# Optimization experiments

Measured on AMD Instinct MI355X. Metric: run time of the kernel, lower is better.

Reference implementation:

```python
import jax, jax.numpy as jnp
import numpy as np

B, S, M = 1, 2048, 2048
H, HKV, D = 32, 8, 64
SW = 128
WAVELENGTH = 150000.0
SCALE = D ** (-0.25)
NEG = -1e9  # large negative for fp32 compute dtype


def setup_inputs() -> dict:
    key = jax.random.key(0)
    ks = jax.random.split(key, 8)
    return {
        "hidden_states": jax.random.normal(ks[0], (B, S, M), jnp.float32),
        "Wq": jax.random.normal(ks[1], (M, H, D), jnp.float32) * 0.02,
        "bq": jnp.zeros((H, D), jnp.float32),
        "Wk": jax.random.normal(ks[2], (M, HKV, D), jnp.float32) * 0.02,
        "bk": jnp.zeros((HKV, D), jnp.float32),
        "Wv": jax.random.normal(ks[3], (M, HKV, D), jnp.float32) * 0.02,
        "bv": jnp.zeros((HKV, D), jnp.float32),
        "Wo": jax.random.normal(ks[4], (H, D, M), jnp.float32) * 0.02,
        "bo": jnp.zeros((M,), jnp.float32),
        "sinks": jax.random.normal(ks[5], (H,), jnp.float32),
    }


def _cos_sin(seq_len, dtype):
    # yarn RoPE with scaling_factor=1.0 reduces to standard RoPE (mscale=1,
    # no frequency interpolation). half = D//2 frequencies.
    half = D // 2
    inv_freq = 1.0 / (WAVELENGTH ** (jnp.arange(half, dtype=jnp.float32) * 2.0 / D))
    t = jnp.arange(seq_len, dtype=jnp.float32)
    freqs = t[:, None] * inv_freq[None, :]  # [S, half]
    # broadcast shape [1, S, 1, half] to match [B, S, heads, half]
    return (jnp.cos(freqs)[None, :, None, :].astype(dtype),
            jnp.sin(freqs)[None, :, None, :].astype(dtype))


def _interleaved_rope(x, cos, sin):
    x_even = x[..., ::2]
    x_odd = x[..., 1::2]
    first = x_even * cos - x_odd * sin
    second = x_odd * cos + x_even * sin
    return jnp.stack([first, second], axis=-1).reshape(x.shape)


def reference(hidden_states, Wq, bq, Wk, bk, Wv, bv, Wo, bo, sinks):
    b, s, _ = hidden_states.shape
    groups = H // HKV

    q = jnp.einsum('bqm,muh->bquh', hidden_states, Wq) + bq  # [B,S,H,D]
    k = jnp.einsum('bkm,mvh->bkvh', hidden_states, Wk) + bk  # [B,S,HKV,D]
    v = jnp.einsum('bkm,mvh->bkvh', hidden_states, Wv) + bv

    cos, sin = _cos_sin(s, hidden_states.dtype)
    q = _interleaved_rope(q, cos, sin) * SCALE
    k = _interleaved_rope(k, cos, sin) * SCALE

    # GQA: repeat kv heads to match query heads
    k = jnp.repeat(k, groups, axis=2)  # [B,S,H,D]
    v = jnp.repeat(v, groups, axis=2)

    scores = jnp.einsum('bquh,bkuh->buqk', q, k)  # [B,H,S,S]

    pos = jnp.arange(s)
    sw_mask = jnp.abs(pos[:, None] - pos[None, :]) <= SW  # bidirectional window
    scores = jnp.where(sw_mask[None, None, :, :], scores, NEG)

    sink_logits = jnp.broadcast_to(sinks[None, :, None, None], (b, H, s, 1))
    combined = jnp.concatenate([scores, sink_logits], axis=-1)  # [B,H,S,S+1]
    probs = jax.nn.softmax(combined.astype(jnp.float32), axis=-1)
    attn = probs[..., :-1].astype(hidden_states.dtype)  # drop sink column

    out = jnp.einsum('buqk,bkuh->bquh', attn, v)  # [B,S,H,D]
    return jnp.einsum('bquh,uhm->bqm', out, Wo) + bo
```

## Files before the change

### kernel.cpp

```cpp
#include <hip/hip_runtime.h>
#include <hip/hip_bf16.h>
#include <stdint.h>

typedef unsigned short u16;
typedef unsigned int   u32;

#define S_LEN 2048
#define NQKV  3072
#define NH    32
#define NKV   8
#define SWIN  128
#define NEGV  (-1.0e9f)
#define SCALE_Q 0.35355339059327379f

typedef __attribute__((ext_vector_type(4)))  float  f32x4;
typedef __attribute__((ext_vector_type(16))) float  f32x16;
typedef __attribute__((ext_vector_type(8)))  __bf16 bf16x8;

__device__ __forceinline__ u16 f2bf(float x){
  u32 u = __float_as_uint(x);
  return (u16)((u + 0x7fffu + ((u >> 16) & 1u)) >> 16);
}
__device__ __forceinline__ float bf2f(u16 h){
  return __uint_as_float(((u32)h) << 16);
}
__device__ __forceinline__ void split2(float a, float b, u32& hw, u32& lw){
  u16 ha = f2bf(a), hb = f2bf(b);
  u16 la = f2bf(a - bf2f(ha)), lb = f2bf(b - bf2f(hb));
  hw = (u32)ha | ((u32)hb << 16);
  lw = (u32)la | ((u32)lb << 16);
}
__device__ __forceinline__ u32 pk2(float a, float b){
  return (u32)f2bf(a) | ((u32)f2bf(b) << 16);
}
__device__ __forceinline__ f32x4 mfma16(bf16x8 a, bf16x8 b, f32x4 c){
  return __builtin_amdgcn_mfma_f32_16x16x32_bf16(a, b, c, 0, 0, 0);
}
__device__ __forceinline__ f32x16 mfma32(bf16x8 a, bf16x8 b, f32x16 c){
  return __builtin_amdgcn_mfma_f32_32x32x16_bf16(a, b, c, 0, 0, 0);
}

typedef __attribute__((address_space(1))) const unsigned int ga_u32;
typedef __attribute__((address_space(3))) unsigned int       ls_u32;
__device__ __forceinline__ void gl16(const void* g, void* l){
  __builtin_amdgcn_global_load_lds((ga_u32*)g, (ls_u32*)l, 16, 0, 0);
}

__global__ __launch_bounds__(256) void k_prep(const float* __restrict__ bq,
                                              const float* __restrict__ bk,
                                              const float* __restrict__ bv,
                                              float* __restrict__ ropetab,
                                              float* __restrict__ bias3){
  int id = blockIdx.x * 256 + threadIdx.x;
  int t = id >> 5, i = id & 31;
  float e = (i * 2.0f) / 64.0f;
  float base = (float)pow(150000.0, (double)e);
  float invf = 1.0f / base;
  float fr = (float)t * invf;
  ropetab[(size_t)id * 2 + 0] = cosf(fr);
  ropetab[(size_t)id * 2 + 1] = sinf(fr);
  if (id < NQKV){
    float b;
    if (id < 2048) b = bq[id];
    else if (id < 2560) b = bk[id - 2048];
    else b = bv[id - 2560];
    bias3[id] = b;
  }
}

__global__ __launch_bounds__(256) void k_pack_a(const float* __restrict__ in,
                                                u16* __restrict__ oh, int n8){
  int id = blockIdx.x * 256 + threadIdx.x;
  if (id >= n8) return;
  int r = id >> 8, p = id & 255;
  const float4* src = (const float4*)(in + (size_t)id * 8);
  float4 v0 = src[0], v1 = src[1];
  u32 hw[4];
  hw[0] = pk2(v0.x, v0.y); hw[1] = pk2(v0.z, v0.w);
  hw[2] = pk2(v1.x, v1.y); hw[3] = pk2(v1.z, v1.w);
  int psw = (p & ~7) | ((p & 7) ^ (r & 7));
  size_t o = ((size_t)r * 256 + psw) * 8;
  *(uint4*)(oh + o) = make_uint4(hw[0], hw[1], hw[2], hw[3]);
}

__global__ __launch_bounds__(256) void k_pack_w(const float* __restrict__ w,
                                                u16* __restrict__ oh,
                                                int K, int N, int NTot, int nOff){
  int id = blockIdx.x * 256 + threadIdx.x;
  int P = K >> 3;
  if (id >= P * N) return;
  int p = id / N, n = id % N;
  u32 hw[4];
  #pragma unroll
  for (int j = 0; j < 4; ++j){
    float a = w[(size_t)(8 * p + 2 * j) * N + n];
    float b = w[(size_t)(8 * p + 2 * j + 1) * N + n];
    hw[j] = pk2(a, b);
  }
  size_t o = ((size_t)p * NTot + nOff + n) * 8;
  *(uint4*)(oh + o) = make_uint4(hw[0], hw[1], hw[2], hw[3]);
}

template<bool ARM>
__global__ __launch_bounds__(256, 2) void k_gemm3(const u16* __restrict__ A,
                                                  const u16* __restrict__ B,
                                                  const float* __restrict__ bias,
                                                  float* __restrict__ C,
                                                  int M, int N, int K){
  __shared__ u16 lds[2][2][1024][8];
  const int tid = threadIdx.x;
  const int lane = tid & 63, wid = tid >> 6;
  const int q = lane & 15, g = lane >> 4;
  const int m0 = blockIdx.y * 128, n0 = blockIdx.x * 128;
  const int wr = wid >> 1, wc = wid & 1;
  const int pkK = K >> 3;

  f32x4 acc[4][4];
  #pragma unroll
  for (int a = 0; a < 4; ++a)
    #pragma unroll
    for (int b = 0; b < 4; ++b)
      #pragma unroll
      for (int r = 0; r < 4; ++r) acc[a][b][r] = 0.0f;

  size_t aoff[4], boff[4];
  #pragma unroll
  for (int c = 0; c < 4; ++c){
    int L = c * 256 + tid;
    if (ARM){
      int row = L >> 3, pa = L & 7;
      aoff[c] = ((size_t)(m0 + row) * pkK + pa) * 8;
    } else {
      int pa = L >> 7, row = L & 127;
      aoff[c] = ((size_t)pa * M + m0 + row) * 8;
    }
    int pb = L >> 7, col = L & 127;
    boff[c] = ((size_t)pb * N + n0 + col) * 8;
  }
  const size_t astep = ARM ? (size_t)64 : (size_t)64 * M;
  const size_t bstep = (size_t)64 * N;

  const int NT = K >> 6;

  auto STAGE = [&](int b){
    #pragma unroll
    for (int c = 0; c < 4; ++c){
      int lbase = c * 256 + wid * 64;
      gl16(A + aoff[c], &lds[b][0][lbase][0]);
      gl16(B + boff[c], &lds[b][1][lbase][0]);
      aoff[c] += astep; boff[c] += bstep;
    }
  };

  STAGE(0);
  STAGE(1);
  asm volatile("s_waitcnt vmcnt(8)" ::: "memory");
  __builtin_amdgcn_s_barrier();

  int buf = 0;
  for (int t = 0; t < NT; ++t){
    bf16x8 af[4][2], bf[4][2];
    #pragma unroll
    for (int ms = 0; ms < 4; ++ms){
      int row = wr * 64 + ms * 16 + q;
      #pragma unroll
      for (int kk = 0; kk < 2; ++kk){
        int ia = ARM ? (row * 8 + ((4 * kk + g) ^ (row & 7)))
                     : ((4 * kk + g) * 128 + row);
        af[ms][kk] = *(const bf16x8*)&lds[buf][0][ia][0];
      }
    }
    #pragma unroll
    for (int ns = 0; ns < 4; ++ns){
      int col = wc * 64 + ns * 16 + q;
      #pragma unroll
      for (int kk = 0; kk < 2; ++kk){
        int ib = (4 * kk + g) * 128 + col;
        bf[ns][kk] = *(const bf16x8*)&lds[buf][1][ib][0];
      }
    }
    asm volatile("s_waitcnt lgkmcnt(0)" ::: "memory");
    __builtin_amdgcn_sched_barrier(0);
    __builtin_amdgcn_s_barrier();
    if (t + 2 < NT) STAGE(buf);

    #pragma unroll
    for (int kk = 0; kk < 2; ++kk)
      #pragma unroll
      for (int ms = 0; ms < 4; ++ms)
        #pragma unroll
        for (int ns = 0; ns < 4; ++ns)
          acc[ms][ns] = mfma16(af[ms][kk], bf[ns][kk], acc[ms][ns]);

    if (t + 2 < NT){
      asm volatile("s_waitcnt vmcnt(8)" ::: "memory");
      __builtin_amdgcn_s_barrier();
    } else if (t + 1 < NT){
      asm volatile("s_waitcnt vmcnt(0)" ::: "memory");
      __builtin_amdgcn_s_barrier();
    }
    buf ^= 1;
  }

  #pragma unroll
  for (int ns = 0; ns < 4; ++ns){
    int col = n0 + wc * 64 + ns * 16 + q;
    float bb = bias[col];
    #pragma unroll
    for (int ms = 0; ms < 4; ++ms){
      int row = m0 + wr * 64 + ms * 16 + g * 4;
      #pragma unroll
      for (int r = 0; r < 4; ++r)
        C[(size_t)(row + r) * N + col] = acc[ms][ns][r] + bb;
    }
  }
}

__global__ __launch_bounds__(256) void k_rope(const float* __restrict__ qkv,
                                              const float* __restrict__ tab,
                                              u16* __restrict__ qoh, u16* __restrict__ qol,
                                              u16* __restrict__ koh, u16* __restrict__ kol){
  const int sL = threadIdx.x & 63, tp = threadIdx.x >> 6;
  const int s = blockIdx.x * 64 + sL;
  int h = blockIdx.y;
  u16* oh; u16* ol; int srcOff;
  if (h < NH){ oh = qoh; ol = qol; srcOff = h * 64; }
  else       { h -= NH; oh = koh; ol = kol; srcOff = 2048 + h * 64; }
  const float4* src = (const float4*)(qkv + (size_t)s * NQKV + srcOff + tp * 16);
  const float4* tb  = (const float4*)(tab + (size_t)s * 64 + tp * 16);
  float xv[16], tv[16];
  #pragma unroll
  for (int i = 0; i < 4; ++i){
    float4 a = src[i]; float4 b = tb[i];
    xv[4*i+0]=a.x; xv[4*i+1]=a.y; xv[4*i+2]=a.z; xv[4*i+3]=a.w;
    tv[4*i+0]=b.x; tv[4*i+1]=b.y; tv[4*i+2]=b.z; tv[4*i+3]=b.w;
  }
  u32 hw[8], lw[8];
  #pragma unroll
  for (int j = 0; j < 8; ++j){
    float e = xv[2*j], o = xv[2*j+1];
    float c = tv[2*j], sn = tv[2*j+1];
    float f0 = (e * c - o * sn) * SCALE_Q;
    float f1 = (o * c + e * sn) * SCALE_Q;
    split2(f0, f1, hw[j], lw[j]);
  }
  size_t o0 = ((size_t)(h * 8 + tp * 2 + 0) * S_LEN + s) * 8;
  size_t o1 = ((size_t)(h * 8 + tp * 2 + 1) * S_LEN + s) * 8;
  *(uint4*)(oh + o0) = make_uint4(hw[0], hw[1], hw[2], hw[3]);
  *(uint4*)(oh + o1) = make_uint4(hw[4], hw[5], hw[6], hw[7]);
  *(uint4*)(ol + o0) = make_uint4(lw[0], lw[1], lw[2], lw[3]);
  *(uint4*)(ol + o1) = make_uint4(lw[4], lw[5], lw[6], lw[7]);
}

__global__ __launch_bounds__(256) void k_split_v2(const float* __restrict__ qkv,
                                                  u16* __restrict__ oh, u16* __restrict__ ol){
  __shared__ float tile[64][65];
  const int h = blockIdx.y;
  const int s0 = blockIdx.x * 64;
  {
    const int sL = threadIdx.x >> 2, ch = threadIdx.x & 3;
    const float4* rp = (const float4*)(qkv + (size_t)(s0 + sL) * NQKV + 2560 + h * 64 + ch * 16);
    #pragma unroll
    for (int i = 0; i < 4; ++i){
      float4 w = rp[i];
      tile[sL][ch * 16 + i * 4 + 0] = w.x;
      tile[sL][ch * 16 + i * 4 + 1] = w.y;
      tile[sL][ch * 16 + i * 4 + 2] = w.z;
      tile[sL][ch * 16 + i * 4 + 3] = w.w;
    }
  }
  __syncthreads();
  const int d = threadIdx.x & 63, spg = threadIdx.x >> 6;
  #pragma unroll
  for (int sp2 = 0; sp2 < 2; ++sp2){
    int spl = spg * 2 + sp2;
    float v[8];
    #pragma unroll
    for (int j = 0; j < 8; ++j) v[j] = tile[spl * 8 + j][d];
    u32 hw[4], lw[4];
    #pragma unroll
    for (int j = 0; j < 4; ++j) split2(v[2*j], v[2*j+1], hw[j], lw[j]);
    size_t o_ = (((size_t)h * 256 + blockIdx.x * 8 + spl) * 64 + d) * 8;
    *(uint4*)(oh + o_) = make_uint4(hw[0], hw[1], hw[2], hw[3]);
    *(uint4*)(ol + o_) = make_uint4(lw[0], lw[1], lw[2], lw[3]);
  }
}

__global__ __launch_bounds__(256) void k_attn(const u16* __restrict__ qh, const u16* __restrict__ ql,
                                              const u16* __restrict__ kh, const u16* __restrict__ kl,
                                              const u16* __restrict__ vh, const u16* __restrict__ vl,
                                              const float* __restrict__ sinks,
                                              u16* __restrict__ aoh){
  const int lane = threadIdx.x & 63;
  const int wid = threadIdx.x >> 6;
  const int h = blockIdx.x;
  const int hkv = h >> 2;
  const int q0 = blockIdx.y * 128 + wid * 32;
  const int lq = lane & 31;
  const int half = lane >> 5;
  const int qi = q0 + lq;

  bf16x8 qfh[4], qfl[4];
  #pragma unroll
  for (int st = 0; st < 4; ++st){
    size_t off = (((size_t)h * 8 + st * 2 + half) * S_LEN + qi) * 8;
    qfh[st] = *(const bf16x8*)(qh + off);
    qfl[st] = *(const bf16x8*)(ql + off);
  }
  float m = sinks[h];
  float lsum = 1.0f;
  f32x16 o0, o1;
  #pragma unroll
  for (int r = 0; r < 16; ++r){ o0[r] = 0.0f; o1[r] = 0.0f; }

  const int kb0 = q0 - 128;
  for (int c = 0; c < 9; ++c){
    const int kb = kb0 + c * 32;
    if (kb + 32 <= 0 || kb >= S_LEN) continue;
    const int keyr = kb + lq;
    const int keyc = min(max(keyr, 0), S_LEN - 1);
    f32x16 sc;
    #pragma unroll
    for (int r = 0; r < 16; ++r) sc[r] = 0.0f;
    #pragma unroll
    for (int st = 0; st < 4; ++st){
      size_t ko = (((size_t)hkv * 8 + st * 2 + half) * S_LEN + keyc) * 8;
      bf16x8 kfh = *(const bf16x8*)(kh + ko);
      bf16x8 kfl = *(const bf16x8*)(kl + ko);
      sc = mfma32(kfh, qfh[st], sc);
      sc = mfma32(kfh, qfl[st], sc);
      sc = mfma32(kfl, qfh[st], sc);
    }
    float tmax = -3.0e38f;
    #pragma unroll
    for (int r = 0; r < 16; ++r){
      int key = kb + (r & 3) + 8 * (r >> 2) + 4 * half;
      int dd = qi - key; if (dd < 0) dd = -dd;
      bool ok = (key >= 0) && (key < S_LEN) && (dd <= SWIN);
      sc[r] = ok ? sc[r] : NEGV;
      tmax = fmaxf(tmax, sc[r]);
    }
    tmax = fmaxf(tmax, __shfl_xor(tmax, 32));
    float mn = fmaxf(m, tmax);
    float alpha = __expf(m - mn);
    m = mn;
    float p[16]; float ps = 0.0f;
    #pragma unroll
    for (int r = 0; r < 16; ++r){ p[r] = __expf(sc[r] - mn); ps += p[r]; }
    ps += __shfl_xor(ps, 32);
    lsum = lsum * alpha + ps;
    #pragma unroll
    for (int r = 0; r < 16; ++r){ o0[r] *= alpha; o1[r] *= alpha; }
    u32 wh[8], wl[8];
    #pragma unroll
    for (int j = 0; j < 8; ++j) split2(p[2 * j], p[2 * j + 1], wh[j], wl[j]);
    bf16x8 pfh[2], pfl[2];
    #pragma unroll
    for (int ks = 0; ks < 2; ++ks){
      u32 x0 = wh[4 * ks + 0], y0 = wh[4 * ks + 2];
      u32 x1 = wh[4 * ks + 1], y1 = wh[4 * ks + 3];
      u32 sx0 = __shfl_xor(x0, 32), sy0 = __shfl_xor(y0, 32);
      u32 sx1 = __shfl_xor(x1, 32), sy1 = __shfl_xor(y1, 32);
      union { u32 u[4]; bf16x8 b; } fb;
      fb.u[0] = half ? sy0 : x0;
      fb.u[1] = half ? sy1 : x1;
      fb.u[2] = half ? y0 : sx0;
      fb.u[3] = half ? y1 : sx1;
      pfh[ks] = fb.b;
      u32 a0 = wl[4 * ks + 0], b0 = wl[4 * ks + 2];
      u32 a1 = wl[4 * ks + 1], b1 = wl[4 * ks + 3];
      u32 sa0 = __shfl_xor(a0, 32), sb0 = __shfl_xor(b0, 32);
      u32 sa1 = __shfl_xor(a1, 32), sb1 = __shfl_xor(b1, 32);
      fb.u[0] = half ? sb0 : a0;
      fb.u[1] = half ? sb1 : a1;
      fb.u[2] = half ? b0 : sa0;
      fb.u[3] = half ? b1 : sa1;
      pfl[ks] = fb.b;
    }
    #pragma unroll
    for (int ks = 0; ks < 2; ++ks){
      int kp = kb / 8 + ks * 2 + half;
      kp = min(max(kp, 0), S_LEN / 8 - 1);
      #pragma unroll
      for (int nt = 0; nt < 2; ++nt){
        size_t vo = (((size_t)hkv * 256 + kp) * 64 + nt * 32 + lq) * 8;
        bf16x8 vfh = *(const bf16x8*)(vh + vo);
        bf16x8 vfl = *(const bf16x8*)(vl + vo);
        f32x16 acc = (nt == 0) ? o0 : o1;
        acc = mfma32(vfh, pfh[ks], acc);
        acc = mfma32(vfh, pfl[ks], acc);
        acc = mfma32(vfl, pfh[ks], acc);
        if (nt == 0) o0 = acc; else o1 = acc;
      }
    }
  }
  float inv = 1.0f / lsum;
  #pragma unroll
  for (int nt = 0; nt < 2; ++nt){
    f32x16 o = (nt == 0) ? o0 : o1;
    #pragma unroll
    for (int rr = 0; rr < 4; ++rr){
      int d0 = nt * 32 + 8 * rr + 4 * half;
      float v0 = o[rr * 4 + 0] * inv, v1 = o[rr * 4 + 1] * inv;
      float v2 = o[rr * 4 + 2] * inv, v3 = o[rr * 4 + 3] * inv;
      int kp_ = h * 8 + nt * 4 + rr;
      size_t oo = ((size_t)kp_ * S_LEN + qi) * 8 + (d0 & 7);
      uint2 wv; wv.x = pk2(v0, v1); wv.y = pk2(v2, v3);
      *(uint2*)(aoh + oo) = wv;
    }
  }
}

extern "C" void kernel_launch(void* const* d_in, const int* in_sizes, int n_in,
                              void* d_out, int out_size, void* d_ws, size_t ws_size,
                              hipStream_t stream){
  const float* hid = (const float*)d_in[0];
  const float* Wq  = (const float*)d_in[1];
  const float* bq  = (const float*)d_in[2];
  const float* Wk  = (const float*)d_in[3];
  const float* bk  = (const float*)d_in[4];
  const float* Wv  = (const float*)d_in[5];
  const float* bv  = (const float*)d_in[6];
  const float* Wo  = (const float*)d_in[7];
  const float* bo  = (const float*)d_in[8];
  const float* sinks = (const float*)d_in[9];
  float* out = (float*)d_out;

  char* w = (char*)d_ws;
  size_t off = 0;
  auto alloc = [&](size_t bytes){ void* p = w + off; off += (bytes + 255) & ~(size_t)255; return p; };
  float* ropetab = (float*)alloc((size_t)S_LEN * 32 * 2 * 4);
  float* bias3   = (float*)alloc((size_t)NQKV * 4);
  u16* Ah  = (u16*)alloc((size_t)2048 * 2048 * 2);
  u16* Bh  = (u16*)alloc((size_t)256 * NQKV * 8 * 2);
  float* QKV = (float*)alloc((size_t)S_LEN * NQKV * 4);
  u16* qph = (u16*)alloc((size_t)NH * 8 * S_LEN * 8 * 2);
  u16* qpl = (u16*)alloc((size_t)NH * 8 * S_LEN * 8 * 2);
  u16* kph = (u16*)alloc((size_t)NKV * 8 * S_LEN * 8 * 2);
  u16* kpl = (u16*)alloc((size_t)NKV * 8 * S_LEN * 8 * 2);
  u16* vph = (u16*)alloc((size_t)NKV * 256 * 64 * 8 * 2);
  u16* vpl = (u16*)alloc((size_t)NKV * 256 * 64 * 8 * 2);
  u16* aoh = (u16*)alloc((size_t)256 * S_LEN * 8 * 2);
  u16* Woh = (u16*)alloc((size_t)256 * 2048 * 8 * 2);
  (void)in_sizes; (void)n_in; (void)out_size; (void)ws_size;

  k_prep<<<256, 256, 0, stream>>>(bq, bk, bv, ropetab, bias3);
  k_pack_a<<<2048, 256, 0, stream>>>(hid, Ah, 2048 * 256);
  k_pack_w<<<2048, 256, 0, stream>>>(Wq, Bh, 2048, 2048, NQKV, 0);
  k_pack_w<<<512, 256, 0, stream>>>(Wk, Bh, 2048, 512, NQKV, 2048);
  k_pack_w<<<512, 256, 0, stream>>>(Wv, Bh, 2048, 512, NQKV, 2560);
  k_pack_w<<<2048, 256, 0, stream>>>(Wo, Woh, 2048, 2048, 2048, 0);
  k_gemm3<true><<<dim3(NQKV / 128, 2048 / 128), 256, 0, stream>>>(Ah, Bh, bias3, QKV,
                                                                  2048, NQKV, 2048);
  k_rope<<<dim3(32, NH + NKV), 256, 0, stream>>>(QKV, ropetab, qph, qpl, kph, kpl);
  k_split_v2<<<dim3(32, NKV), 256, 0, stream>>>(QKV, vph, vpl);
  k_attn<<<dim3(NH, S_LEN / 128), 256, 0, stream>>>(qph, qpl, kph, kpl, vph, vpl, sinks, aoh);
  k_gemm3<false><<<dim3(2048 / 128, 2048 / 128), 256, 0, stream>>>(aoh, Woh, bo, out,
                                                                   2048, 2048, 2048);
}
```

Measured before the change: 217.5 us.

## Drop split-bf16 hi/lo compensation in attention and merge packing kernels

Measured after the change: 201.8 us. 7.2% less time.

```diff
diff --git a/kernel.cpp b/kernel.cpp
--- a/kernel.cpp
+++ b/kernel.cpp
@@ -20,15 +20,6 @@
 __device__ __forceinline__ u16 f2bf(float x){
   u32 u = __float_as_uint(x);
   return (u16)((u + 0x7fffu + ((u >> 16) & 1u)) >> 16);
-}
-__device__ __forceinline__ float bf2f(u16 h){
-  return __uint_as_float(((u32)h) << 16);
-}
-__device__ __forceinline__ void split2(float a, float b, u32& hw, u32& lw){
-  u16 ha = f2bf(a), hb = f2bf(b);
-  u16 la = f2bf(a - bf2f(ha)), lb = f2bf(b - bf2f(hb));
-  hw = (u32)ha | ((u32)hb << 16);
-  lw = (u32)la | ((u32)lb << 16);
 }
 __device__ __forceinline__ u32 pk2(float a, float b){
   return (u32)f2bf(a) | ((u32)f2bf(b) << 16);
@@ -68,27 +59,9 @@
   }
 }
 
-__global__ __launch_bounds__(256) void k_pack_a(const float* __restrict__ in,
-                                                u16* __restrict__ oh, int n8){
-  int id = blockIdx.x * 256 + threadIdx.x;
-  if (id >= n8) return;
-  int r = id >> 8, p = id & 255;
-  const float4* src = (const float4*)(in + (size_t)id * 8);
-  float4 v0 = src[0], v1 = src[1];
-  u32 hw[4];
-  hw[0] = pk2(v0.x, v0.y); hw[1] = pk2(v0.z, v0.w);
-  hw[2] = pk2(v1.x, v1.y); hw[3] = pk2(v1.z, v1.w);
-  int psw = (p & ~7) | ((p & 7) ^ (r & 7));
-  size_t o = ((size_t)r * 256 + psw) * 8;
-  *(uint4*)(oh + o) = make_uint4(hw[0], hw[1], hw[2], hw[3]);
-}
-
-__global__ __launch_bounds__(256) void k_pack_w(const float* __restrict__ w,
-                                                u16* __restrict__ oh,
-                                                int K, int N, int NTot, int nOff){
-  int id = blockIdx.x * 256 + threadIdx.x;
-  int P = K >> 3;
-  if (id >= P * N) return;
+__device__ __forceinline__ void packw_seg(const float* __restrict__ w,
+                                          u16* __restrict__ oh,
+                                          int N, int NTot, int nOff, int id){
   int p = id / N, n = id % N;
   u32 hw[4];
   #pragma unroll
@@ -99,6 +72,36 @@
   }
   size_t o = ((size_t)p * NTot + nOff + n) * 8;
   *(uint4*)(oh + o) = make_uint4(hw[0], hw[1], hw[2], hw[3]);
+}
+__global__ __launch_bounds__(256) void k_packall(const float* __restrict__ hid,
+                                                 const float* __restrict__ Wq,
+                                                 const float* __restrict__ Wk,
+                                                 const float* __restrict__ Wv,
+                                                 const float* __restrict__ Wo,
+                                                 u16* __restrict__ Ah,
+                                                 u16* __restrict__ Bh,
+                                                 u16* __restrict__ Woh){
+  int b = blockIdx.x;
+  if (b < 2048){
+    int id = b * 256 + threadIdx.x;
+    int r = id >> 8, p = id & 255;
+    const float4* src = (const float4*)(hid + (size_t)id * 8);
+    float4 v0 = src[0], v1 = src[1];
+    u32 hw[4];
+    hw[0] = pk2(v0.x, v0.y); hw[1] = pk2(v0.z, v0.w);
+    hw[2] = pk2(v1.x, v1.y); hw[3] = pk2(v1.z, v1.w);
+    int psw = (p & ~7) | ((p & 7) ^ (r & 7));
+    size_t o = ((size_t)r * 256 + psw) * 8;
+    *(uint4*)(Ah + o) = make_uint4(hw[0], hw[1], hw[2], hw[3]);
+  } else if (b < 4096){
+    packw_seg(Wq, Bh, 2048, NQKV, 0,    (b - 2048) * 256 + threadIdx.x);
+  } else if (b < 4608){
+    packw_seg(Wk, Bh, 512,  NQKV, 2048, (b - 4096) * 256 + threadIdx.x);
+  } else if (b < 5120){
+    packw_seg(Wv, Bh, 512,  NQKV, 2560, (b - 4608) * 256 + threadIdx.x);
+  } else {
+    packw_seg(Wo, Woh, 2048, 2048, 0,   (b - 5120) * 256 + threadIdx.x);
+  }
 }
 
 template<bool ARM>
@@ -218,14 +221,14 @@
 
 __global__ __launch_bounds__(256) void k_rope(const float* __restrict__ qkv,
                                               const float* __restrict__ tab,
-                                              u16* __restrict__ qoh, u16* __restrict__ qol,
-                                              u16* __restrict__ koh, u16* __restrict__ kol){
+                                              u16* __restrict__ qoh,
+                                              u16* __restrict__ koh){
   const int sL = threadIdx.x & 63, tp = threadIdx.x >> 6;
   const int s = blockIdx.x * 64 + sL;
   int h = blockIdx.y;
-  u16* oh; u16* ol; int srcOff;
-  if (h < NH){ oh = qoh; ol = qol; srcOff = h * 64; }
-  else       { h -= NH; oh = koh; ol = kol; srcOff = 2048 + h * 64; }
+  u16* oh; int srcOff;
+  if (h < NH){ oh = qoh; srcOff = h * 64; }
+  else       { h -= NH; oh = koh; srcOff = 2048 + h * 64; }
   const float4* src = (const float4*)(qkv + (size_t)s * NQKV + srcOff + tp * 16);
   const float4* tb  = (const float4*)(tab + (size_t)s * 64 + tp * 16);
   float xv[16], tv[16];
@@ -235,25 +238,23 @@
     xv[4*i+0]=a.x; xv[4*i+1]=a.y; xv[4*i+2]=a.z; xv[4*i+3]=a.w;
     tv[4*i+0]=b.x; tv[4*i+1]=b.y; tv[4*i+2]=b.z; tv[4*i+3]=b.w;
   }
-  u32 hw[8], lw[8];
+  u32 hw[8];
   #pragma unroll
   for (int j = 0; j < 8; ++j){
     float e = xv[2*j], o = xv[2*j+1];
     float c = tv[2*j], sn = tv[2*j+1];
     float f0 = (e * c - o * sn) * SCALE_Q;
     float f1 = (o * c + e * sn) * SCALE_Q;
-    split2(f0, f1, hw[j], lw[j]);
+    hw[j] = pk2(f0, f1);
   }
   size_t o0 = ((size_t)(h * 8 + tp * 2 + 0) * S_LEN + s) * 8;
   size_t o1 = ((size_t)(h * 8 + tp * 2 + 1) * S_LEN + s) * 8;
   *(uint4*)(oh + o0) = make_uint4(hw[0], hw[1], hw[2], hw[3]);
   *(uint4*)(oh + o1) = make_uint4(hw[4], hw[5], hw[6], hw[7]);
-  *(uint4*)(ol + o0) = make_uint4(lw[0], lw[1], lw[2], lw[3]);
-  *(uint4*)(ol + o1) = make_uint4(lw[4], lw[5], lw[6], lw[7]);
 }
 
 __global__ __launch_bounds__(256) void k_split_v2(const float* __restrict__ qkv,
-                                                  u16* __restrict__ oh, u16* __restrict__ ol){
+                                                  u16* __restrict__ oh){
   __shared__ float tile[64][65];
   const int h = blockIdx.y;
   const int s0 = blockIdx.x * 64;
@@ -277,18 +278,17 @@
     float v[8];
     #pragma unroll
     for (int j = 0; j < 8; ++j) v[j] = tile[spl * 8 + j][d];
-    u32 hw[4], lw[4];
-    #pragma unroll
-    for (int j = 0; j < 4; ++j) split2(v[2*j], v[2*j+1], hw[j], lw[j]);
+    u32 hw[4];
+    #pragma unroll
+    for (int j = 0; j < 4; ++j) hw[j] = pk2(v[2*j], v[2*j+1]);
     size_t o_ = (((size_t)h * 256 + blockIdx.x * 8 + spl) * 64 + d) * 8;
     *(uint4*)(oh + o_) = make_uint4(hw[0], hw[1], hw[2], hw[3]);
-    *(uint4*)(ol + o_) = make_uint4(lw[0], lw[1], lw[2], lw[3]);
-  }
-}
-
-__global__ __launch_bounds__(256) void k_attn(const u16* __restrict__ qh, const u16* __restrict__ ql,
-                                              const u16* __restrict__ kh, const u16* __restrict__ kl,
-                                              const u16* __restrict__ vh, const u16* __restrict__ vl,
+  }
+}
+
+__global__ __launch_bounds__(256) void k_attn(const u16* __restrict__ qh,
+                                              const u16* __restrict__ kh,
+                                              const u16* __restrict__ vh,
                                               const float* __restrict__ sinks,
                                               u16* __restrict__ aoh){
   const int lane = threadIdx.x & 63;
@@ -300,12 +300,11 @@
   const int half = lane >> 5;
   const int qi = q0 + lq;
 
-  bf16x8 qfh[4], qfl[4];
+  bf16x8 qf[4];
   #pragma unroll
   for (int st = 0; st < 4; ++st){
     size_t off = (((size_t)h * 8 + st * 2 + half) * S_LEN + qi) * 8;
-    qfh[st] = *(const bf16x8*)(qh + off);
-    qfl[st] = *(const bf16x8*)(ql + off);
+    qf[st] = *(const bf16x8*)(qh + off);
   }
   float m = sinks[h];
   float lsum = 1.0f;
@@ -325,11 +324,8 @@
     #pragma unroll
     for (int st = 0; st < 4; ++st){
       size_t ko = (((size_t)hkv * 8 + st * 2 + half) * S_LEN + keyc) * 8;
-      bf16x8 kfh = *(const bf16x8*)(kh + ko);
-      bf16x8 kfl = *(const bf16x8*)(kl + ko);
-      sc = mfma32(kfh, qfh[st], sc);
-      sc = mfma32(kfh, qfl[st], sc);
-      sc = mfma32(kfl, qfh[st], sc);
+      bf16x8 kf = *(const bf16x8*)(kh + ko);
+      sc = mfma32(kf, qf[st], sc);
     }
     float tmax = -3.0e38f;
     #pragma unroll
@@ -351,10 +347,10 @@
     lsum = lsum * alpha + ps;
     #pragma unroll
     for (int r = 0; r < 16; ++r){ o0[r] *= alpha; o1[r] *= alpha; }
-    u32 wh[8], wl[8];
-    #pragma unroll
-    for (int j = 0; j < 8; ++j) split2(p[2 * j], p[2 * j + 1], wh[j], wl[j]);
-    bf16x8 pfh[2], pfl[2];
+    u32 wh[8];
+    #pragma unroll
+    for (int j = 0; j < 8; ++j) wh[j] = pk2(p[2 * j], p[2 * j + 1]);
+    bf16x8 pfh[2];
     #pragma unroll
     for (int ks = 0; ks < 2; ++ks){
       u32 x0 = wh[4 * ks + 0], y0 = wh[4 * ks + 2];
@@ -367,15 +363,6 @@
       fb.u[2] = half ? y0 : sx0;
       fb.u[3] = half ? y1 : sx1;
       pfh[ks] = fb.b;
-      u32 a0 = wl[4 * ks + 0], b0 = wl[4 * ks + 2];
-      u32 a1 = wl[4 * ks + 1], b1 = wl[4 * ks + 3];
-      u32 sa0 = __shfl_xor(a0, 32), sb0 = __shfl_xor(b0, 32);
-      u32 sa1 = __shfl_xor(a1, 32), sb1 = __shfl_xor(b1, 32);
-      fb.u[0] = half ? sb0 : a0;
-      fb.u[1] = half ? sb1 : a1;
-      fb.u[2] = half ? b0 : sa0;
-      fb.u[3] = half ? b1 : sa1;
-      pfl[ks] = fb.b;
     }
     #pragma unroll
     for (int ks = 0; ks < 2; ++ks){
@@ -384,12 +371,9 @@
       #pragma unroll
       for (int nt = 0; nt < 2; ++nt){
         size_t vo = (((size_t)hkv * 256 + kp) * 64 + nt * 32 + lq) * 8;
-        bf16x8 vfh = *(const bf16x8*)(vh + vo);
-        bf16x8 vfl = *(const bf16x8*)(vl + vo);
+        bf16x8 vf = *(const bf16x8*)(vh + vo);
         f32x16 acc = (nt == 0) ? o0 : o1;
-        acc = mfma32(vfh, pfh[ks], acc);
-        acc = mfma32(vfh, pfl[ks], acc);
-        acc = mfma32(vfl, pfh[ks], acc);
+        acc = mfma32(vf, pfh[ks], acc);
         if (nt == 0) o0 = acc; else o1 = acc;
       }
     }
@@ -435,26 +419,19 @@
   u16* Bh  = (u16*)alloc((size_t)256 * NQKV * 8 * 2);
   float* QKV = (float*)alloc((size_t)S_LEN * NQKV * 4);
   u16* qph = (u16*)alloc((size_t)NH * 8 * S_LEN * 8 * 2);
-  u16* qpl = (u16*)alloc((size_t)NH * 8 * S_LEN * 8 * 2);
   u16* kph = (u16*)alloc((size_t)NKV * 8 * S_LEN * 8 * 2);
-  u16* kpl = (u16*)alloc((size_t)NKV * 8 * S_LEN * 8 * 2);
   u16* vph = (u16*)alloc((size_t)NKV * 256 * 64 * 8 * 2);
-  u16* vpl = (u16*)alloc((size_t)NKV * 256 * 64 * 8 * 2);
   u16* aoh = (u16*)alloc((size_t)256 * S_LEN * 8 * 2);
   u16* Woh = (u16*)alloc((size_t)256 * 2048 * 8 * 2);
   (void)in_sizes; (void)n_in; (void)out_size; (void)ws_size;
 
   k_prep<<<256, 256, 0, stream>>>(bq, bk, bv, ropetab, bias3);
-  k_pack_a<<<2048, 256, 0, stream>>>(hid, Ah, 2048 * 256);
-  k_pack_w<<<2048, 256, 0, stream>>>(Wq, Bh, 2048, 2048, NQKV, 0);
-  k_pack_w<<<512, 256, 0, stream>>>(Wk, Bh, 2048, 512, NQKV, 2048);
-  k_pack_w<<<512, 256, 0, stream>>>(Wv, Bh, 2048, 512, NQKV, 2560);
-  k_pack_w<<<2048, 256, 0, stream>>>(Wo, Woh, 2048, 2048, 2048, 0);
+  k_packall<<<7168, 256, 0, stream>>>(hid, Wq, Wk, Wv, Wo, Ah, Bh, Woh);
   k_gemm3<true><<<dim3(NQKV / 128, 2048 / 128), 256, 0, stream>>>(Ah, Bh, bias3, QKV,
                                                                   2048, NQKV, 2048);
-  k_rope<<<dim3(32, NH + NKV), 256, 0, stream>>>(QKV, ropetab, qph, qpl, kph, kpl);
-  k_split_v2<<<dim3(32, NKV), 256, 0, stream>>>(QKV, vph, vpl);
-  k_attn<<<dim3(NH, S_LEN / 128), 256, 0, stream>>>(qph, qpl, kph, kpl, vph, vpl, sinks, aoh);
+  k_rope<<<dim3(32, NH + NKV), 256, 0, stream>>>(QKV, ropetab, qph, kph);
+  k_split_v2<<<dim3(32, NKV), 256, 0, stream>>>(QKV, vph);
+  k_attn<<<dim3(NH, S_LEN / 128), 256, 0, stream>>>(qph, kph, vph, sinks, aoh);
   k_gemm3<false><<<dim3(2048 / 128, 2048 / 128), 256, 0, stream>>>(aoh, Woh, bo, out,
                                                                    2048, 2048, 2048);
 }
```
